# Optimization experiments

Hardware: AMD Instinct MI355X
Metric: run time of the kernel (lower is better)

The kernel has to match this reference:

```python
import jax, jax.numpy as jnp
import numpy as np

NEG_SLOPE = 0.01  # nn.LeakyReLU default


def setup_inputs() -> dict:
    key = jax.random.key(0)
    k1, k2, k3, k4, k5, k6 = jax.random.split(key, 6)
    N, E, F_IN, F_OUT = 50000, 800000, 256, 64
    x = jax.random.normal(k1, (N, F_IN), dtype=jnp.float32)
    src = jax.random.randint(k2, (E,), 0, N, dtype=jnp.int32)
    dst = jax.random.randint(k3, (E,), 0, N, dtype=jnp.int32)
    # nn.init.normal_(weight, 0, 0.5) for both Linear layers (no bias)
    W1 = 0.5 * jax.random.normal(k4, (F_OUT, F_IN), dtype=jnp.float32)
    W2 = 0.5 * jax.random.normal(k5, (F_OUT, F_OUT), dtype=jnp.float32)
    # detGAT.a = torch.rand(2*out_feats, 1)
    a = jax.random.uniform(k6, (2 * F_OUT, 1), dtype=jnp.float32)
    return {"x": x, "W1": W1, "W2": W2, "a": a, "src": src, "dst": dst}


def reference(x, W1, W2, a, src, dst):
    N, d = x.shape[0], W1.shape[0]
    # model_base: linear -> (dropout, identity in eval) -> relu, twice
    z = jax.nn.relu(x @ W1.T)
    h = jax.nn.relu(z @ W2.T)  # [N, d]
    # detGAT edge score: LeakyReLU(concat([h_dst, h_src]) @ a)
    # split a so we compute per-node dot products once instead of an [E, 2d] concat
    a_dst, a_src = a[:d, 0], a[d:, 0]
    s_dst = h @ a_dst  # [N]
    s_src = h @ a_src  # [N]
    score = jax.nn.leaky_relu(s_dst[dst] + s_src[src], NEG_SLOPE)  # [E]
    # edge_softmax: softmax over incoming edges of each destination node
    m = jax.ops.segment_max(score, dst, num_segments=N)  # [N]
    e = jnp.exp(score - m[dst])
    ssum = jax.ops.segment_sum(e, dst, num_segments=N)  # [N]
    w = e / ssum[dst]  # [E]
    # weighted scatter-sum of src features to dst nodes
    res = jax.ops.segment_sum(h[src] * w[:, None], dst, num_segments=N)  # [N, d]
    return jax.nn.relu(h - res)
```

## Files before the change

### kernel.cpp

```cpp
#include <hip/hip_runtime.h>
#include <math.h>

#define F_IN 256
#define F_OUT 64
#define NEG_SLOPE 0.01f
#define CAP 8192
#define NB2 256

typedef unsigned short ushort8_t __attribute__((ext_vector_type(8)));
typedef __bf16 bf16x8 __attribute__((ext_vector_type(8)));
typedef float f32x16 __attribute__((ext_vector_type(16)));

__device__ inline unsigned short f2bf(float f) {
    unsigned u = __float_as_uint(f);
    u += 0x7FFF + ((u >> 16) & 1);
    return (unsigned short)(u >> 16);
}
__device__ inline float bf2f(unsigned short u) {
    return __uint_as_float(((unsigned)u) << 16);
}
__device__ inline void splitbf(float x, unsigned short& hi, unsigned short& lo) {
    hi = f2bf(x);
    lo = f2bf(x - bf2f(hi));
}
__device__ inline bf16x8 asbf8(ushort8_t u) {
    union { ushort8_t u; bf16x8 b; } c; c.u = u; return c.b;
}
__device__ inline float redq32(float v) {
    v += __shfl_xor(v, 1);  v += __shfl_xor(v, 2);  v += __shfl_xor(v, 4);
    v += __shfl_xor(v, 8);  v += __shfl_xor(v, 16);
    return v;
}

__global__ __launch_bounds__(1024)
void prep_scatter_kernel(const float* __restrict__ W1, const float* __restrict__ W2,
                         unsigned short* __restrict__ w1fh, unsigned short* __restrict__ w1fl,
                         unsigned short* __restrict__ w2fh, unsigned short* __restrict__ w2fl,
                         const int* __restrict__ src, const int* __restrict__ dst,
                         int* __restrict__ cursor, int* __restrict__ edata,
                         int E, int chunk)
{
    __shared__ int lh[256], lbase[256], lcur[256];
    const int tid = threadIdx.x;

    if (blockIdx.x < 16) {
        int idx = blockIdx.x * 1024 + tid;
        int jj = idx & 7, l = (idx >> 3) & 63, t = idx >> 9;
        {
            int nt = t & 1, gks = t >> 1;
            int f = nt * 32 + (l & 31);
            int k = gks * 16 + (l >> 5) * 8 + jj;
            unsigned short hi, lo;
            splitbf(W1[f * F_IN + k], hi, lo);
            w1fh[idx] = hi; w1fl[idx] = lo;
        }
        if (idx < 4096) {
            int nt = t & 1, ks = t >> 1;
            int f = nt * 32 + (l & 31);
            int j = ks * 16 + (l >> 5) * 8 + jj;
            unsigned short hi, lo;
            splitbf(W2[f * F_OUT + j], hi, lo);
            w2fh[idx] = hi; w2fl[idx] = lo;
        }
        return;
    }

    const int bid = blockIdx.x - 16;
    if (tid < 256) lh[tid] = 0;
    __syncthreads();
    const int beg = bid * chunk;
    const int end = min(E, beg + chunk);
    for (int i = beg + tid; i < end; i += 1024)
        atomicAdd(&lh[((unsigned)dst[i]) >> 8], 1);
    __syncthreads();
    if (tid < 256) {
        int c = lh[tid];
        lbase[tid] = c ? atomicAdd(&cursor[tid], c) : 0;
        lcur[tid] = 0;
    }
    __syncthreads();
    for (int i = beg + tid; i < end; i += 1024) {
        int d = dst[i];
        int s = src[i];
        int b = ((unsigned)d) >> 8;
        int rk = atomicAdd(&lcur[b], 1);
        edata[b * CAP + lbase[b] + rk] = ((d & 0xFF) << 16) | s;
    }
}

__global__ __launch_bounds__(256, 2)
void mlp_sort_kernel(const float* __restrict__ x,
                     const unsigned short* __restrict__ w1fh,
                     const unsigned short* __restrict__ w1fl,
                     const unsigned short* __restrict__ w2fh,
                     const unsigned short* __restrict__ w2fl,
                     const float* __restrict__ a,
                     unsigned short* __restrict__ hb,
                     float* __restrict__ sdst,
                     float* __restrict__ ssrc, int N,
                     const int* __restrict__ cursor,
                     const int* __restrict__ edata,
                     int* __restrict__ ssorted,
                     int* __restrict__ cnt, int* __restrict__ offs,
                     int MLPB)
{
    __shared__ __align__(16) unsigned short zbuf[4 * 8576];
    __shared__ int hist[256];
    __shared__ int excl[256];

    const int tid = threadIdx.x;
    const int lane = tid & 63;

    if (blockIdx.x < MLPB) {
        const int wid = __builtin_amdgcn_readfirstlane(tid >> 6);
        const int ml = lane & 31;
        const int q = lane >> 5;
        const int hl = lane >> 5;
        const int cl = lane & 31;
        const int node0w = blockIdx.x * 128 + wid * 32;

        unsigned short* xh = zbuf + wid * 8576;
        unsigned short* xl = xh + 4288;
        unsigned short* zh = xh;
        unsigned short* zl = xh + 2112;

        f32x16 acc0, acc1;
#pragma unroll
        for (int i = 0; i < 16; i++) { acc0[i] = 0.f; acc1[i] = 0.f; }

#pragma unroll
        for (int half = 0; half < 2; half++) {
            float4 v[16];
#pragma unroll
            for (int i = 0; i < 16; i++) {
                int r = 2 * i + hl;
                int rr = min(node0w + r, N - 1);
                v[i] = *(const float4*)(x + (size_t)rr * F_IN + half * 128 + cl * 4);
            }
#pragma unroll
            for (int i = 0; i < 16; i++) {
                int r = 2 * i + hl;
                ushort4 h4, l4;
                unsigned short th, tl;
                splitbf(v[i].x, th, tl); h4.x = th; l4.x = tl;
                splitbf(v[i].y, th, tl); h4.y = th; l4.y = tl;
                splitbf(v[i].z, th, tl); h4.z = th; l4.z = tl;
                splitbf(v[i].w, th, tl); h4.w = th; l4.w = tl;
                *(ushort4*)(xh + r * 134 + cl * 4) = h4;
                *(ushort4*)(xl + r * 134 + cl * 4) = l4;
            }
#pragma unroll
            for (int ks = 0; ks < 8; ks++) {
                int gks = half * 8 + ks;
                bf16x8 ah = asbf8(*(const ushort8_t*)(xh + ml * 134 + ks * 16 + q * 8));
                bf16x8 al = asbf8(*(const ushort8_t*)(xl + ml * 134 + ks * 16 + q * 8));
                bf16x8 bh0 = asbf8(*(const ushort8_t*)(w1fh + ((gks * 2 + 0) * 64 + lane) * 8));
                bf16x8 bl0 = asbf8(*(const ushort8_t*)(w1fl + ((gks * 2 + 0) * 64 + lane) * 8));
                bf16x8 bh1 = asbf8(*(const ushort8_t*)(w1fh + ((gks * 2 + 1) * 64 + lane) * 8));
                bf16x8 bl1 = asbf8(*(const ushort8_t*)(w1fl + ((gks * 2 + 1) * 64 + lane) * 8));
                acc0 = __builtin_amdgcn_mfma_f32_32x32x16_bf16(ah, bh0, acc0, 0, 0, 0);
                acc0 = __builtin_amdgcn_mfma_f32_32x32x16_bf16(ah, bl0, acc0, 0, 0, 0);
                acc0 = __builtin_amdgcn_mfma_f32_32x32x16_bf16(al, bh0, acc0, 0, 0, 0);
                acc1 = __builtin_amdgcn_mfma_f32_32x32x16_bf16(ah, bh1, acc1, 0, 0, 0);
                acc1 = __builtin_amdgcn_mfma_f32_32x32x16_bf16(ah, bl1, acc1, 0, 0, 0);
                acc1 = __builtin_amdgcn_mfma_f32_32x32x16_bf16(al, bh1, acc1, 0, 0, 0);
            }
        }

#pragma unroll
        for (int reg = 0; reg < 16; reg++) {
            int nd = (reg & 3) + 8 * (reg >> 2) + 4 * q;
            float z0 = fmaxf(acc0[reg], 0.f);
            float z1 = fmaxf(acc1[reg], 0.f);
            unsigned short h_, l_;
            splitbf(z0, h_, l_);
            zh[nd * 66 + ml] = h_; zl[nd * 66 + ml] = l_;
            splitbf(z1, h_, l_);
            zh[nd * 66 + 32 + ml] = h_; zl[nd * 66 + 32 + ml] = l_;
        }

        f32x16 hacc0, hacc1;
#pragma unroll
        for (int i = 0; i < 16; i++) { hacc0[i] = 0.f; hacc1[i] = 0.f; }
#pragma unroll
        for (int ks = 0; ks < 4; ks++) {
            bf16x8 wh0 = asbf8(*(const ushort8_t*)(w2fh + ((ks * 2 + 0) * 64 + lane) * 8));
            bf16x8 wl0 = asbf8(*(const ushort8_t*)(w2fl + ((ks * 2 + 0) * 64 + lane) * 8));
            bf16x8 wh1 = asbf8(*(const ushort8_t*)(w2fh + ((ks * 2 + 1) * 64 + lane) * 8));
            bf16x8 wl1 = asbf8(*(const ushort8_t*)(w2fl + ((ks * 2 + 1) * 64 + lane) * 8));
            bf16x8 ah = asbf8(*(const ushort8_t*)(zh + ml * 66 + ks * 16 + q * 8));
            bf16x8 al = asbf8(*(const ushort8_t*)(zl + ml * 66 + ks * 16 + q * 8));
            hacc0 = __builtin_amdgcn_mfma_f32_32x32x16_bf16(ah, wh0, hacc0, 0, 0, 0);
            hacc0 = __builtin_amdgcn_mfma_f32_32x32x16_bf16(ah, wl0, hacc0, 0, 0, 0);
            hacc0 = __builtin_amdgcn_mfma_f32_32x32x16_bf16(al, wh0, hacc0, 0, 0, 0);
            hacc1 = __builtin_amdgcn_mfma_f32_32x32x16_bf16(ah, wh1, hacc1, 0, 0, 0);
            hacc1 = __builtin_amdgcn_mfma_f32_32x32x16_bf16(ah, wl1, hacc1, 0, 0, 0);
            hacc1 = __builtin_amdgcn_mfma_f32_32x32x16_bf16(al, wh1, hacc1, 0, 0, 0);
        }

        const float aD0 = a[ml],            aD1 = a[32 + ml];
        const float aS0 = a[F_OUT + ml],    aS1 = a[F_OUT + 32 + ml];

        float sdv = 0.f, ssv = 0.f;
#pragma unroll
        for (int reg = 0; reg < 16; reg++) {
            int nd = (reg & 3) + 8 * (reg >> 2) + 4 * q;
            float h0 = fmaxf(hacc0[reg], 0.f);
            float h1 = fmaxf(hacc1[reg], 0.f);
            float td = redq32(h0 * aD0 + h1 * aD1);
            float ts = redq32(h0 * aS0 + h1 * aS1);
            if (ml == nd) { sdv = td; ssv = ts; }
            int gn = node0w + nd;
            if (gn < N) {
                hb[(size_t)gn * F_OUT + ml]      = f2bf(h0);
                hb[(size_t)gn * F_OUT + 32 + ml] = f2bf(h1);
            }
        }
        {
            int gn = node0w + ml;
            if ((((ml >> 2) & 1) == q) && gn < N) {
                sdst[gn] = sdv;
                ssrc[gn] = ssv;
            }
        }
        return;
    }

    const int cb = blockIdx.x - MLPB;
    const int base = cb * CAP;
    const int ecnt = cursor[cb];

    hist[tid] = 0;
    __syncthreads();
    for (int i = tid; i < ecnt; i += 256)
        atomicAdd(&hist[((unsigned)edata[base + i]) >> 16], 1);
    __syncthreads();

    if (tid < 64) {
        int v0 = hist[lane * 4], v1 = hist[lane * 4 + 1];
        int v2 = hist[lane * 4 + 2], v3 = hist[lane * 4 + 3];
        int ts = v0 + v1 + v2 + v3;
        int s = ts;
#pragma unroll
        for (int d = 1; d < 64; d <<= 1) {
            int t = __shfl_up(s, d);
            if (lane >= d) s += t;
        }
        int e = s - ts;
        excl[lane * 4] = e;
        excl[lane * 4 + 1] = e + v0;
        excl[lane * 4 + 2] = e + v0 + v1;
        excl[lane * 4 + 3] = e + v0 + v1 + v2;
    }
    __syncthreads();

    {
        int d = cb * 256 + tid;
        if (d < N) {
            cnt[d] = hist[tid];
            offs[d] = base + excl[tid];
        }
    }
    __syncthreads();

    for (int i = tid; i < ecnt; i += 256) {
        int pack = edata[base + i];
        int low = ((unsigned)pack) >> 16;
        int rk = atomicAdd(&excl[low], 1);
        ssorted[base + rk] = pack & 0xFFFF;
    }
}

__global__ __launch_bounds__(256)
void aggregate_kernel(const unsigned short* __restrict__ hb,
                      const float* __restrict__ sdst,
                      const float* __restrict__ ssrc,
                      const int* __restrict__ offs,
                      const int* __restrict__ cnt,
                      const int* __restrict__ ssorted,
                      float* __restrict__ out, int N)
{
    __shared__ float2 ws_sh[4][64];
    const int tid = threadIdx.x;
    const int lane = tid & 63;
    const int wid = tid >> 6;
    const int g = lane >> 4;
    const int li = lane & 15;
    const int d = blockIdx.x * 16 + wid * 4 + g;
    const bool vd = d < N;

    const int off = vd ? offs[d] : 0;
    const int deg = vd ? cnt[d] : 0;
    const float sdd = vd ? sdst[d] : 0.f;

    float M = -INFINITY, S = 0.f;
    float c0 = 0.f, c1 = 0.f, c2 = 0.f, c3 = 0.f;

    for (int cb = 0; cb < deg; cb += 16) {
        int ce = min(16, deg - cb);
        float score = -INFINITY;
        int s = 0;
        if (li < ce) {
            s = ssorted[off + cb + li];
            float sc = sdd + ssrc[s];
            score = sc > 0.f ? sc : NEG_SLOPE * sc;
        }
        float mc = score;
        mc = fmaxf(mc, __shfl_xor(mc, 1));
        mc = fmaxf(mc, __shfl_xor(mc, 2));
        mc = fmaxf(mc, __shfl_xor(mc, 4));
        mc = fmaxf(mc, __shfl_xor(mc, 8));
        float newM = fmaxf(M, mc);
        float scale = __expf(M - newM);
        float w = (li < ce) ? __expf(score - newM) : 0.f;
        ws_sh[wid][lane] = make_float2(w, __int_as_float(s));
        float csum = w;
        csum += __shfl_xor(csum, 1);
        csum += __shfl_xor(csum, 2);
        csum += __shfl_xor(csum, 4);
        csum += __shfl_xor(csum, 8);
        S = S * scale + csum;
        __builtin_amdgcn_wave_barrier();

        float t0 = 0.f, t1 = 0.f, t2 = 0.f, t3 = 0.f;
#pragma unroll
        for (int e = 0; e < 16; e++) {
            float2 tw = ws_sh[wid][g * 16 + e];
            int se = __float_as_int(tw.y);
            ushort4 r = *(const ushort4*)(hb + (((size_t)(unsigned)se) << 6) + li * 4);
            t0 = fmaf(tw.x, bf2f(r.x), t0);
            t1 = fmaf(tw.x, bf2f(r.y), t1);
            t2 = fmaf(tw.x, bf2f(r.z), t2);
            t3 = fmaf(tw.x, bf2f(r.w), t3);
        }
        c0 = c0 * scale + t0;
        c1 = c1 * scale + t1;
        c2 = c2 * scale + t2;
        c3 = c3 * scale + t3;
        __builtin_amdgcn_wave_barrier();
        M = newM;
    }

    if (vd) {
        ushort4 hr = *(const ushort4*)(hb + (((size_t)(unsigned)d) << 6) + li * 4);
        float inv = (S > 0.f) ? 1.f / S : 0.f;
        float r0 = bf2f(hr.x) - c0 * inv;
        float r1 = bf2f(hr.y) - c1 * inv;
        float r2 = bf2f(hr.z) - c2 * inv;
        float r3 = bf2f(hr.w) - c3 * inv;
        float4 o;
        o.x = r0 > 0.f ? r0 : 0.f;
        o.y = r1 > 0.f ? r1 : 0.f;
        o.z = r2 > 0.f ? r2 : 0.f;
        o.w = r3 > 0.f ? r3 : 0.f;
        *(float4*)(out + (size_t)d * F_OUT + li * 4) = o;
    }
}

extern "C" void kernel_launch(void* const* d_in, const int* in_sizes, int n_in,
                              void* d_out, int out_size, void* d_ws,
                              size_t ws_size, hipStream_t stream)
{
    const float* x  = (const float*)d_in[0];
    const float* W1 = (const float*)d_in[1];
    const float* W2 = (const float*)d_in[2];
    const float* a  = (const float*)d_in[3];
    const int* src  = (const int*)d_in[4];
    const int* dst  = (const int*)d_in[5];
    const int N = in_sizes[0] / F_IN;
    const int E = in_sizes[4];

    float* ws = (float*)d_ws;
    float* sdst = ws;
    float* ssrc = sdst + N;
    unsigned short* w1fh = (unsigned short*)(ssrc + N);
    unsigned short* w1fl = w1fh + 16384;
    unsigned short* w2fh = w1fl + 16384;
    unsigned short* w2fl = w2fh + 4096;
    unsigned short* hb = w2fl + 4096;
    int* cnt    = (int*)(hb + (size_t)N * F_OUT);
    int* offs   = cnt + N;
    int* cursor = offs + N;
    int* edata  = cursor + 256;
    int* ssorted = edata + 196 * CAP;

    const int nbc = (N + 255) >> 8;
    const int MLPB = (N + 127) >> 7;
    const int chunk = (E + NB2 - 1) / NB2;

    hipMemsetAsync(cursor, 0, 256 * sizeof(int), stream);
    prep_scatter_kernel<<<16 + NB2, 1024, 0, stream>>>(W1, W2, w1fh, w1fl, w2fh, w2fl,
                                                       src, dst, cursor, edata, E, chunk);
    mlp_sort_kernel<<<MLPB + nbc, 256, 0, stream>>>(x, w1fh, w1fl, w2fh, w2fl, a,
                                                    hb, sdst, ssrc, N,
                                                    cursor, edata, ssorted, cnt, offs,
                                                    MLPB);
    aggregate_kernel<<<(N + 15) / 16, 256, 0, stream>>>(hb, sdst, ssrc, offs, cnt,
                                                        ssorted, (float*)d_out, N);
}
```

Measured before the change: 147.9 us.

## Restructure pipeline: overlap edge scatter with MLP and fuse sort into aggregation

The bucket scatter of edges moves into the MLP kernel, with MLP and scatter blocks interleaved so they run together, and the memset is folded into the weight-prep kernel. The per-bucket counting sort is fused with aggregation in a 1024-thread block that keeps sorted source indices in LDS, which removes the global ssorted/cnt/offs arrays and one kernel launch. In exchange the aggregation grid shrinks to about 196 large blocks, which may lower parallelism for the gather-heavy phase.

```diff
diff --git a/kernel.cpp b/kernel.cpp
--- a/kernel.cpp
+++ b/kernel.cpp
@@ -5,7 +5,7 @@
 #define F_OUT 64
 #define NEG_SLOPE 0.01f
 #define CAP 8192
-#define NB2 256
+#define SB 512
 
 typedef unsigned short ushort8_t __attribute__((ext_vector_type(8)));
 typedef __bf16 bf16x8 __attribute__((ext_vector_type(8)));
@@ -32,92 +32,69 @@
     return v;
 }
 
-__global__ __launch_bounds__(1024)
-void prep_scatter_kernel(const float* __restrict__ W1, const float* __restrict__ W2,
-                         unsigned short* __restrict__ w1fh, unsigned short* __restrict__ w1fl,
-                         unsigned short* __restrict__ w2fh, unsigned short* __restrict__ w2fl,
-                         const int* __restrict__ src, const int* __restrict__ dst,
-                         int* __restrict__ cursor, int* __restrict__ edata,
-                         int E, int chunk)
+__global__ __launch_bounds__(256)
+void prep_kernel(const float* __restrict__ W1, const float* __restrict__ W2,
+                 unsigned short* __restrict__ w1fh, unsigned short* __restrict__ w1fl,
+                 unsigned short* __restrict__ w2fh, unsigned short* __restrict__ w2fl,
+                 int* __restrict__ cursor)
 {
-    __shared__ int lh[256], lbase[256], lcur[256];
-    const int tid = threadIdx.x;
-
-    if (blockIdx.x < 16) {
-        int idx = blockIdx.x * 1024 + tid;
-        int jj = idx & 7, l = (idx >> 3) & 63, t = idx >> 9;
-        {
-            int nt = t & 1, gks = t >> 1;
-            int f = nt * 32 + (l & 31);
-            int k = gks * 16 + (l >> 5) * 8 + jj;
-            unsigned short hi, lo;
-            splitbf(W1[f * F_IN + k], hi, lo);
-            w1fh[idx] = hi; w1fl[idx] = lo;
-        }
-        if (idx < 4096) {
-            int nt = t & 1, ks = t >> 1;
-            int f = nt * 32 + (l & 31);
-            int j = ks * 16 + (l >> 5) * 8 + jj;
-            unsigned short hi, lo;
-            splitbf(W2[f * F_OUT + j], hi, lo);
-            w2fh[idx] = hi; w2fl[idx] = lo;
-        }
-        return;
-    }
-
-    const int bid = blockIdx.x - 16;
-    if (tid < 256) lh[tid] = 0;
-    __syncthreads();
-    const int beg = bid * chunk;
-    const int end = min(E, beg + chunk);
-    for (int i = beg + tid; i < end; i += 1024)
-        atomicAdd(&lh[((unsigned)dst[i]) >> 8], 1);
-    __syncthreads();
-    if (tid < 256) {
-        int c = lh[tid];
-        lbase[tid] = c ? atomicAdd(&cursor[tid], c) : 0;
-        lcur[tid] = 0;
-    }
-    __syncthreads();
-    for (int i = beg + tid; i < end; i += 1024) {
-        int d = dst[i];
-        int s = src[i];
-        int b = ((unsigned)d) >> 8;
-        int rk = atomicAdd(&lcur[b], 1);
-        edata[b * CAP + lbase[b] + rk] = ((d & 0xFF) << 16) | s;
+    int idx = blockIdx.x * 256 + threadIdx.x;
+    if (blockIdx.x == 0) cursor[threadIdx.x] = 0;
+    int jj = idx & 7, l = (idx >> 3) & 63, t = idx >> 9;
+    {
+        int nt = t & 1, gks = t >> 1;
+        int f = nt * 32 + (l & 31);
+        int k = gks * 16 + (l >> 5) * 8 + jj;
+        unsigned short hi, lo;
+        splitbf(W1[f * F_IN + k], hi, lo);
+        w1fh[idx] = hi; w1fl[idx] = lo;
+    }
+    if (idx < 4096) {
+        int nt = t & 1, ks = t >> 1;
+        int f = nt * 32 + (l & 31);
+        int j = ks * 16 + (l >> 5) * 8 + jj;
+        unsigned short hi, lo;
+        splitbf(W2[f * F_OUT + j], hi, lo);
+        w2fh[idx] = hi; w2fl[idx] = lo;
     }
 }
 
 __global__ __launch_bounds__(256, 2)
-void mlp_sort_kernel(const float* __restrict__ x,
-                     const unsigned short* __restrict__ w1fh,
-                     const unsigned short* __restrict__ w1fl,
-                     const unsigned short* __restrict__ w2fh,
-                     const unsigned short* __restrict__ w2fl,
-                     const float* __restrict__ a,
-                     unsigned short* __restrict__ hb,
-                     float* __restrict__ sdst,
-                     float* __restrict__ ssrc, int N,
-                     const int* __restrict__ cursor,
-                     const int* __restrict__ edata,
-                     int* __restrict__ ssorted,
-                     int* __restrict__ cnt, int* __restrict__ offs,
-                     int MLPB)
+void mlp_scatter_kernel(const float* __restrict__ x,
+                        const unsigned short* __restrict__ w1fh,
+                        const unsigned short* __restrict__ w1fl,
+                        const unsigned short* __restrict__ w2fh,
+                        const unsigned short* __restrict__ w2fl,
+                        const float* __restrict__ a,
+                        unsigned short* __restrict__ hb,
+                        float* __restrict__ sdst,
+                        float* __restrict__ ssrc, int N,
+                        const int* __restrict__ src, const int* __restrict__ dst,
+                        int* __restrict__ cursor, int* __restrict__ edata,
+                        int E, int chunk, int MLPB)
 {
     __shared__ __align__(16) unsigned short zbuf[4 * 8576];
-    __shared__ int hist[256];
-    __shared__ int excl[256];
 
     const int tid = threadIdx.x;
     const int lane = tid & 63;
-
-    if (blockIdx.x < MLPB) {
+    const int bid = blockIdx.x;
+
+    int mbid, sbid;
+    if (bid < 2 * MLPB) {
+        mbid = ((bid & 1) == 0) ? (bid >> 1) : -1;
+        sbid = ((bid & 1) == 1) ? (bid >> 1) : -1;
+    } else {
+        mbid = -1;
+        sbid = bid - MLPB;
+    }
+
+    if (mbid >= 0) {
         const int wid = __builtin_amdgcn_readfirstlane(tid >> 6);
         const int ml = lane & 31;
         const int q = lane >> 5;
         const int hl = lane >> 5;
         const int cl = lane & 31;
-        const int node0w = blockIdx.x * 128 + wid * 32;
+        const int node0w = mbid * 128 + wid * 32;
 
         unsigned short* xh = zbuf + wid * 8576;
         unsigned short* xl = xh + 4288;
@@ -226,13 +203,55 @@
         return;
     }
 
-    const int cb = blockIdx.x - MLPB;
+    int* lh = (int*)zbuf;
+    int* lbase = lh + 256;
+    int* lcur = lh + 512;
+    lh[tid] = 0;
+    __syncthreads();
+    const int beg = sbid * chunk;
+    const int end = min(E, beg + chunk);
+    for (int i = beg + tid; i < end; i += 256)
+        atomicAdd(&lh[((unsigned)dst[i]) >> 8], 1);
+    __syncthreads();
+    {
+        int c = lh[tid];
+        lbase[tid] = c ? atomicAdd(&cursor[tid], c) : 0;
+        lcur[tid] = 0;
+    }
+    __syncthreads();
+    for (int i = beg + tid; i < end; i += 256) {
+        int d = dst[i];
+        int s = src[i];
+        int b = ((unsigned)d) >> 8;
+        int rk = atomicAdd(&lcur[b], 1);
+        edata[b * CAP + lbase[b] + rk] = ((d & 0xFF) << 16) | s;
+    }
+}
+
+__global__ __launch_bounds__(1024)
+void sortagg_kernel(const int* __restrict__ cursor,
+                    const int* __restrict__ edata,
+                    const unsigned short* __restrict__ hb,
+                    const float* __restrict__ sdst,
+                    const float* __restrict__ ssrc,
+                    float* __restrict__ out, int N)
+{
+    __shared__ int hist[256];
+    __shared__ int excl[256];
+    __shared__ int start_s[256];
+    __shared__ unsigned short ssl[CAP];
+    __shared__ float2 ws_sh[16][64];
+
+    const int tid = threadIdx.x;
+    const int lane = tid & 63;
+    const int wid = tid >> 6;
+    const int cb = blockIdx.x;
     const int base = cb * CAP;
     const int ecnt = cursor[cb];
 
-    hist[tid] = 0;
-    __syncthreads();
-    for (int i = tid; i < ecnt; i += 256)
+    if (tid < 256) hist[tid] = 0;
+    __syncthreads();
+    for (int i = tid; i < ecnt; i += 1024)
         atomicAdd(&hist[((unsigned)edata[base + i]) >> 16], 1);
     __syncthreads();
 
@@ -253,107 +272,91 @@
         excl[lane * 4 + 3] = e + v0 + v1 + v2;
     }
     __syncthreads();
-
-    {
-        int d = cb * 256 + tid;
-        if (d < N) {
-            cnt[d] = hist[tid];
-            offs[d] = base + excl[tid];
-        }
-    }
-    __syncthreads();
-
-    for (int i = tid; i < ecnt; i += 256) {
+    if (tid < 256) start_s[tid] = excl[tid];
+    __syncthreads();
+
+    for (int i = tid; i < ecnt; i += 1024) {
         int pack = edata[base + i];
         int low = ((unsigned)pack) >> 16;
         int rk = atomicAdd(&excl[low], 1);
-        ssorted[base + rk] = pack & 0xFFFF;
-    }
-}
-
-__global__ __launch_bounds__(256)
-void aggregate_kernel(const unsigned short* __restrict__ hb,
-                      const float* __restrict__ sdst,
-                      const float* __restrict__ ssrc,
-                      const int* __restrict__ offs,
-                      const int* __restrict__ cnt,
-                      const int* __restrict__ ssorted,
-                      float* __restrict__ out, int N)
-{
-    __shared__ float2 ws_sh[4][64];
-    const int tid = threadIdx.x;
-    const int lane = tid & 63;
-    const int wid = tid >> 6;
+        ssl[rk] = (unsigned short)(pack & 0xFFFF);
+    }
+    __syncthreads();
+
     const int g = lane >> 4;
     const int li = lane & 15;
-    const int d = blockIdx.x * 16 + wid * 4 + g;
-    const bool vd = d < N;
-
-    const int off = vd ? offs[d] : 0;
-    const int deg = vd ? cnt[d] : 0;
-    const float sdd = vd ? sdst[d] : 0.f;
-
-    float M = -INFINITY, S = 0.f;
-    float c0 = 0.f, c1 = 0.f, c2 = 0.f, c3 = 0.f;
-
-    for (int cb = 0; cb < deg; cb += 16) {
-        int ce = min(16, deg - cb);
-        float score = -INFINITY;
-        int s = 0;
-        if (li < ce) {
-            s = ssorted[off + cb + li];
-            float sc = sdd + ssrc[s];
-            score = sc > 0.f ? sc : NEG_SLOPE * sc;
-        }
-        float mc = score;
-        mc = fmaxf(mc, __shfl_xor(mc, 1));
-        mc = fmaxf(mc, __shfl_xor(mc, 2));
-        mc = fmaxf(mc, __shfl_xor(mc, 4));
-        mc = fmaxf(mc, __shfl_xor(mc, 8));
-        float newM = fmaxf(M, mc);
-        float scale = __expf(M - newM);
-        float w = (li < ce) ? __expf(score - newM) : 0.f;
-        ws_sh[wid][lane] = make_float2(w, __int_as_float(s));
-        float csum = w;
-        csum += __shfl_xor(csum, 1);
-        csum += __shfl_xor(csum, 2);
-        csum += __shfl_xor(csum, 4);
-        csum += __shfl_xor(csum, 8);
-        S = S * scale + csum;
-        __builtin_amdgcn_wave_barrier();
-
-        float t0 = 0.f, t1 = 0.f, t2 = 0.f, t3 = 0.f;
-#pragma unroll
-        for (int e = 0; e < 16; e++) {
-            float2 tw = ws_sh[wid][g * 16 + e];
-            int se = __float_as_int(tw.y);
-            ushort4 r = *(const ushort4*)(hb + (((size_t)(unsigned)se) << 6) + li * 4);
-            t0 = fmaf(tw.x, bf2f(r.x), t0);
-            t1 = fmaf(tw.x, bf2f(r.y), t1);
-            t2 = fmaf(tw.x, bf2f(r.z), t2);
-            t3 = fmaf(tw.x, bf2f(r.w), t3);
-        }
-        c0 = c0 * scale + t0;
-        c1 = c1 * scale + t1;
-        c2 = c2 * scale + t2;
-        c3 = c3 * scale + t3;
-        __builtin_amdgcn_wave_barrier();
-        M = newM;
-    }
-
-    if (vd) {
-        ushort4 hr = *(const ushort4*)(hb + (((size_t)(unsigned)d) << 6) + li * 4);
-        float inv = (S > 0.f) ? 1.f / S : 0.f;
-        float r0 = bf2f(hr.x) - c0 * inv;
-        float r1 = bf2f(hr.y) - c1 * inv;
-        float r2 = bf2f(hr.z) - c2 * inv;
-        float r3 = bf2f(hr.w) - c3 * inv;
-        float4 o;
-        o.x = r0 > 0.f ? r0 : 0.f;
-        o.y = r1 > 0.f ? r1 : 0.f;
-        o.z = r2 > 0.f ? r2 : 0.f;
-        o.w = r3 > 0.f ? r3 : 0.f;
-        *(float4*)(out + (size_t)d * F_OUT + li * 4) = o;
+    const int grp = wid * 4 + g;
+
+    for (int rep = 0; rep < 4; rep++) {
+        const int local = rep * 64 + grp;
+        const int d = cb * 256 + local;
+        const bool vd = d < N;
+        const int off = vd ? start_s[local] : 0;
+        const int deg = vd ? hist[local] : 0;
+        const float sdd = vd ? sdst[d] : 0.f;
+
+        float M = -INFINITY, S = 0.f;
+        float c0 = 0.f, c1 = 0.f, c2 = 0.f, c3 = 0.f;
+
+        for (int ch = 0; ch < deg; ch += 16) {
+            int ce = min(16, deg - ch);
+            float score = -INFINITY;
+            int s = 0;
+            if (li < ce) {
+                s = ssl[off + ch + li];
+                float sc = sdd + ssrc[s];
+                score = sc > 0.f ? sc : NEG_SLOPE * sc;
+            }
+            float mc = score;
+            mc = fmaxf(mc, __shfl_xor(mc, 1));
+            mc = fmaxf(mc, __shfl_xor(mc, 2));
+            mc = fmaxf(mc, __shfl_xor(mc, 4));
+            mc = fmaxf(mc, __shfl_xor(mc, 8));
+            float newM = fmaxf(M, mc);
+            float scale = __expf(M - newM);
+            float w = (li < ce) ? __expf(score - newM) : 0.f;
+            ws_sh[wid][lane] = make_float2(w, __int_as_float(s));
+            float csum = w;
+            csum += __shfl_xor(csum, 1);
+            csum += __shfl_xor(csum, 2);
+            csum += __shfl_xor(csum, 4);
+            csum += __shfl_xor(csum, 8);
+            S = S * scale + csum;
+            __builtin_amdgcn_wave_barrier();
+
+            float t0 = 0.f, t1 = 0.f, t2 = 0.f, t3 = 0.f;
+#pragma unroll
+            for (int e = 0; e < 16; e++) {
+                float2 tw = ws_sh[wid][g * 16 + e];
+                int se = __float_as_int(tw.y);
+                ushort4 r = *(const ushort4*)(hb + (((size_t)(unsigned)se) << 6) + li * 4);
+                t0 = fmaf(tw.x, bf2f(r.x), t0);
+                t1 = fmaf(tw.x, bf2f(r.y), t1);
+                t2 = fmaf(tw.x, bf2f(r.z), t2);
+                t3 = fmaf(tw.x, bf2f(r.w), t3);
+            }
+            c0 = c0 * scale + t0;
+            c1 = c1 * scale + t1;
+            c2 = c2 * scale + t2;
+            c3 = c3 * scale + t3;
+            __builtin_amdgcn_wave_barrier();
+            M = newM;
+        }
+
+        if (vd) {
+            ushort4 hr = *(const ushort4*)(hb + (((size_t)(unsigned)d) << 6) + li * 4);
+            float inv = (S > 0.f) ? 1.f / S : 0.f;
+            float r0 = bf2f(hr.x) - c0 * inv;
+            float r1 = bf2f(hr.y) - c1 * inv;
+            float r2 = bf2f(hr.z) - c2 * inv;
+            float r3 = bf2f(hr.w) - c3 * inv;
+            float4 o;
+            o.x = r0 > 0.f ? r0 : 0.f;
+            o.y = r1 > 0.f ? r1 : 0.f;
+            o.z = r2 > 0.f ? r2 : 0.f;
+            o.w = r3 > 0.f ? r3 : 0.f;
+            *(float4*)(out + (size_t)d * F_OUT + li * 4) = o;
+        }
     }
 }
 
@@ -378,23 +381,18 @@
     unsigned short* w2fh = w1fl + 16384;
     unsigned short* w2fl = w2fh + 4096;
     unsigned short* hb = w2fl + 4096;
-    int* cnt    = (int*)(hb + (size_t)N * F_OUT);
-    int* offs   = cnt + N;
-    int* cursor = offs + N;
+    int* cursor = (int*)(hb + (size_t)N * F_OUT);
     int* edata  = cursor + 256;
-    int* ssorted = edata + 196 * CAP;
 
     const int nbc = (N + 255) >> 8;
     const int MLPB = (N + 127) >> 7;
-    const int chunk = (E + NB2 - 1) / NB2;
-
-    hipMemsetAsync(cursor, 0, 256 * sizeof(int), stream);
-    prep_scatter_kernel<<<16 + NB2, 1024, 0, stream>>>(W1, W2, w1fh, w1fl, w2fh, w2fl,
-                                                       src, dst, cursor, edata, E, chunk);
-    mlp_sort_kernel<<<MLPB + nbc, 256, 0, stream>>>(x, w1fh, w1fl, w2fh, w2fl, a,
-                                                    hb, sdst, ssrc, N,
-                                                    cursor, edata, ssorted, cnt, offs,
-                                                    MLPB);
-    aggregate_kernel<<<(N + 15) / 16, 256, 0, stream>>>(hb, sdst, ssrc, offs, cnt,
-                                                        ssorted, (float*)d_out, N);
-}
+    const int chunk = (E + SB - 1) / SB;
+
+    prep_kernel<<<64, 256, 0, stream>>>(W1, W2, w1fh, w1fl, w2fh, w2fl, cursor);
+    mlp_scatter_kernel<<<MLPB + SB, 256, 0, stream>>>(x, w1fh, w1fl, w2fh, w2fl, a,
+                                                      hb, sdst, ssrc, N,
+                                                      src, dst, cursor, edata,
+                                                      E, chunk, MLPB);
+    sortagg_kernel<<<nbc, 1024, 0, stream>>>(cursor, edata, hb, sdst, ssrc,
+                                             (float*)d_out, N);
+}
```

Result: slower. 161.6 us (+9.3%).
